# Optimization experiments

Measured on AMD Instinct MI355X. Metric: run time of the kernel, lower is better.

## Reference

```python
import jax, jax.numpy as jnp
import numpy as np
from jax.scipy.linalg import solve_triangular

CHUNK = 64

def _l2norm(x, eps=1e-6):
    return x * jax.lax.rsqrt(jnp.sum(x * x, axis=-1, keepdims=True) + eps)

def setup_inputs() -> dict:
    key = jax.random.key(0)
    ks = jax.random.split(key, 5)
    B, S, H, Dk, Dv = 2, 4096, 16, 128, 128
    query = jax.random.normal(ks[0], (B, S, H, Dk), jnp.float32)
    key_t = jax.random.normal(ks[1], (B, S, H, Dk), jnp.float32)
    value = jax.random.normal(ks[2], (B, S, H, Dv), jnp.float32)
    # g is a log-decay gate: must be <= 0 so exp(cumsum(g)) stays bounded
    g = -0.1 * jax.random.uniform(ks[3], (B, S, H), jnp.float32)
    beta = jax.random.uniform(ks[4], (B, S, H), jnp.float32)
    return {"query": query, "key": key_t, "value": value, "g": g, "beta": beta}

def reference(query, key, value, g, beta):
    """Chunked gated delta rule (faithful to torch_chunk_gated_delta_rule).
    query/key: [B,S,H,Dk], value: [B,S,H,Dv], g/beta: [B,S,H]."""
    dtype0 = query.dtype
    q = _l2norm(query).transpose(0, 2, 1, 3).astype(jnp.float32)  # [B,H,S,Dk]
    k = _l2norm(key).transpose(0, 2, 1, 3).astype(jnp.float32)
    v = value.transpose(0, 2, 1, 3).astype(jnp.float32)           # [B,H,S,Dv]
    b = beta.transpose(0, 2, 1).astype(jnp.float32)               # [B,H,S]
    gl = g.transpose(0, 2, 1).astype(jnp.float32)
    B, H, S, Dk = k.shape
    Dv = v.shape[-1]
    pad = (-S) % CHUNK
    if pad:
        q = jnp.pad(q, ((0, 0), (0, 0), (0, pad), (0, 0)))
        k = jnp.pad(k, ((0, 0), (0, 0), (0, pad), (0, 0)))
        v = jnp.pad(v, ((0, 0), (0, 0), (0, pad), (0, 0)))
        b = jnp.pad(b, ((0, 0), (0, 0), (0, pad)))
        gl = jnp.pad(gl, ((0, 0), (0, 0), (0, pad)))
    N = (S + pad) // CHUNK
    q = q * (Dk ** -0.5)
    vb = v * b[..., None]
    kb = k * b[..., None]
    qc = q.reshape(B, H, N, CHUNK, Dk)
    kc = k.reshape(B, H, N, CHUNK, Dk)
    vc = vb.reshape(B, H, N, CHUNK, Dv)
    kbc = kb.reshape(B, H, N, CHUNK, Dk)
    gc = gl.reshape(B, H, N, CHUNK)
    gcs = jnp.cumsum(gc, axis=-1)                                  # within-chunk cum log-decay
    tri = jnp.tril(jnp.ones((CHUNK, CHUNK), bool))                 # incl diag
    tri_strict = jnp.tril(jnp.ones((CHUNK, CHUNK), bool), -1)
    # decay[i,j] = exp(g_i - g_j) for i >= j else 0
    decay = jnp.where(tri, jnp.exp(jnp.where(tri, gcs[..., :, None] - gcs[..., None, :], 0.0)), 0.0)
    # Torch builds T = (I + strict_lower(k_beta k^T * decay))^{-1} via forward substitution;
    # same result from a unit-lower triangular solve.
    A = jnp.where(tri_strict, jnp.einsum('bhnck,bhndk->bhncd', kbc, kc) * decay, 0.0)
    M = A + jnp.eye(CHUNK, dtype=A.dtype)
    eye = jnp.broadcast_to(jnp.eye(CHUNK, dtype=A.dtype), M.shape)
    Tinv = solve_triangular(M, eye, lower=True, unit_diagonal=True)
    u = jnp.einsum('bhncd,bhndv->bhncv', Tinv, vc)                 # attn @ v_beta
    kcd = jnp.einsum('bhncd,bhndk->bhnck', Tinv, kbc * jnp.exp(gcs)[..., None])  # k_cumdecay

    def step(state, xs):
        q_i, k_i, u_i, kcd_i, g_i, dec_i = xs                      # [B,H,C,*]
        attn = jnp.where(tri, jnp.einsum('bhck,bhdk->bhcd', q_i, k_i) * dec_i, 0.0)
        v_new = u_i - jnp.einsum('bhck,bhkv->bhcv', kcd_i, state)
        o_i = jnp.einsum('bhck,bhkv->bhcv', q_i * jnp.exp(g_i)[..., None], state) \
            + jnp.einsum('bhcd,bhdv->bhcv', attn, v_new)
        g_last = g_i[..., -1]                                      # [B,H]
        k_dec = k_i * jnp.exp(g_last[..., None] - g_i)[..., None]
        state = state * jnp.exp(g_last)[..., None, None] \
            + jnp.einsum('bhck,bhcv->bhkv', k_dec, v_new)
        return state, o_i

    xs = tuple(jnp.moveaxis(a, 2, 0) for a in (qc, kc, u, kcd, gcs, decay))
    state0 = jnp.zeros((B, H, Dk, Dv), jnp.float32)
    _, out = jax.lax.scan(step, state0, xs)                        # out: [N,B,H,C,Dv]
    out = jnp.moveaxis(out, 0, 2).reshape(B, H, N * CHUNK, Dv)[:, :, :S]
    return out.transpose(0, 2, 1, 3).astype(dtype0)                # [B,S,H,Dv]
```

## Files before the change

### kernel.cpp

```cpp
#include <hip/hip_runtime.h>
#include <hip/hip_fp16.h>

#define B_   2
#define S_   4096
#define H_   16
#define DK_  128
#define DV_  128
#define CK_  64
#define NC_  (S_/CK_)
#define QSCALE 0.08838834764831845f

#define DOT4(a,b) ((a).x*(b).x + (a).y*(b).y + (a).z*(b).z + (a).w*(b).w)

#define SWH(c, r) (((((c) >> 3) ^ (((r) >> 2) & 7)) << 3) | ((c) & 7))
#define SWV(c, r) (((((c) >> 2) ^ (((r) >> 2) & 7)) << 2) | ((c) & 3))

static __device__ __forceinline__ unsigned short f2bf(float x) {
    unsigned u = __float_as_uint(x);
    unsigned r = u + 0x7fffu + ((u >> 16) & 1u);
    return (unsigned short)(r >> 16);
}
static __device__ __forceinline__ float bf2f(unsigned short h) {
    return __uint_as_float(((unsigned)h) << 16);
}
static __device__ __forceinline__ float4 h4tof4(const __half* p) {
    float2 f01 = __half22float2(*(const __half2*)p);
    float2 f23 = __half22float2(*(const __half2*)(p + 2));
    return make_float4(f01.x, f01.y, f23.x, f23.y);
}
static __device__ __forceinline__ void f4toh4(__half* p, float4 v) {
    *(__half2*)p       = __floats2half2_rn(v.x, v.y);
    *(__half2*)(p + 2) = __floats2half2_rn(v.z, v.w);
}

struct f8 { float4 lo, hi; };
static __device__ __forceinline__ f8 unp_bf16x8(uint4 u) {
    f8 r;
    r.lo.x = __uint_as_float(u.x << 16); r.lo.y = __uint_as_float(u.x & 0xffff0000u);
    r.lo.z = __uint_as_float(u.y << 16); r.lo.w = __uint_as_float(u.y & 0xffff0000u);
    r.hi.x = __uint_as_float(u.z << 16); r.hi.y = __uint_as_float(u.z & 0xffff0000u);
    r.hi.z = __uint_as_float(u.w << 16); r.hi.w = __uint_as_float(u.w & 0xffff0000u);
    return r;
}
static __device__ __forceinline__ f8 unp_f16x8(uint4 u) {
    f8 r;
    float2 a = __half22float2(*(__half2*)&u.x), b = __half22float2(*(__half2*)&u.y);
    float2 c = __half22float2(*(__half2*)&u.z), d = __half22float2(*(__half2*)&u.w);
    r.lo = make_float4(a.x, a.y, b.x, b.y);
    r.hi = make_float4(c.x, c.y, d.x, d.y);
    return r;
}

__global__ __launch_bounds__(256) void dr_phase1(
    const float* __restrict__ Q, const float* __restrict__ K,
    const float* __restrict__ V, const float* __restrict__ G,
    const float* __restrict__ Bt,
    unsigned short* __restrict__ Uw, unsigned short* __restrict__ KCDw,
    unsigned short* __restrict__ ATTNw,
    float* __restrict__ RQw, float* __restrict__ RKw, float* __restrict__ EGw)
{
    __shared__ float kn[64][132];
    __shared__ __align__(16) __half bufh[64][136];
    __shared__ float T[64][68];
    __shared__ float tmp[32][36];
    __shared__ float bet[64], rn[64], epos[64], eneg[64], cL[64], cR[64];

    const int tid = threadIdx.x;
    const int cid = blockIdx.x;
    const int n   = cid & (NC_ - 1);
    const int bh  = cid >> 6;
    const int h   = bh & (H_ - 1);
    const int b   = bh >> 4;
    const int rowbase = (b*S_ + n*CK_)*H_ + h;

    #pragma unroll
    for (int i = 0; i < 8; ++i) {
        int idx4 = tid + 256*i;
        int r = idx4 >> 5, c0 = (idx4 & 31) << 2;
        *(float4*)&kn[r][c0 ^ (r & 28)] =
            *(const float4*)(K + (size_t)(rowbase + r*H_)*DK_ + c0);
    }
    if (tid < 64) {
        float g = G[rowbase + tid*H_];
        #pragma unroll
        for (int off = 1; off < 64; off <<= 1) {
            float o = __shfl_up(g, off, 64);
            if (tid >= off) g += o;
        }
        float ep = expf(g);
        epos[tid] = ep;
        eneg[tid] = expf(-g);
        bet[tid]  = Bt[rowbase + tid*H_];
        if (tid == 63) EGw[cid] = ep;
    }
    __syncthreads();

    #pragma unroll
    for (int i = 0; i < 8; ++i) {
        int idx4 = tid + 256*i;
        int r = idx4 >> 5, c0 = (idx4 & 31) << 2;
        float bb = bet[r];
        float4 vv = *(const float4*)(V + (size_t)(rowbase + r*H_)*DV_ + c0);
        vv.x *= bb; vv.y *= bb; vv.z *= bb; vv.w *= bb;
        f4toh4(&bufh[r][c0], vv);
    }
    if (tid < 64) {
        const int xr = tid & 28;
        float s = 0.f;
        #pragma unroll
        for (int c = 0; c < 128; c += 4) { float4 x = *(float4*)&kn[tid][c ^ xr]; s += DOT4(x,x); }
        float r_ = rsqrtf(s + 1e-6f);
        rn[tid] = r_;
        RKw[cid*64 + tid] = r_*epos[63]*eneg[tid];
        cL[tid] = bet[tid]*epos[tid]*r_;
        cR[tid] = eneg[tid]*r_;
    }
    __syncthreads();

    {
        const int i0 = (tid >> 4) << 2, j0 = (tid & 15) << 2;
        const int xi = i0 & 28, xj = j0 & 28;
        float acc[4][4] = {};
        if (j0 <= i0) {
            for (int c = 0; c < 128; c += 4) {
                float4 a0 = *(float4*)&kn[i0  ][c ^ xi], a1 = *(float4*)&kn[i0+1][c ^ xi];
                float4 a2 = *(float4*)&kn[i0+2][c ^ xi], a3 = *(float4*)&kn[i0+3][c ^ xi];
                float4 b0 = *(float4*)&kn[j0  ][c ^ xj], b1 = *(float4*)&kn[j0+1][c ^ xj];
                float4 b2 = *(float4*)&kn[j0+2][c ^ xj], b3 = *(float4*)&kn[j0+3][c ^ xj];
                acc[0][0]+=DOT4(a0,b0); acc[0][1]+=DOT4(a0,b1); acc[0][2]+=DOT4(a0,b2); acc[0][3]+=DOT4(a0,b3);
                acc[1][0]+=DOT4(a1,b0); acc[1][1]+=DOT4(a1,b1); acc[1][2]+=DOT4(a1,b2); acc[1][3]+=DOT4(a1,b3);
                acc[2][0]+=DOT4(a2,b0); acc[2][1]+=DOT4(a2,b1); acc[2][2]+=DOT4(a2,b2); acc[2][3]+=DOT4(a2,b3);
                acc[3][0]+=DOT4(a3,b0); acc[3][1]+=DOT4(a3,b1); acc[3][2]+=DOT4(a3,b2); acc[3][3]+=DOT4(a3,b3);
            }
        }
        #pragma unroll
        for (int x = 0; x < 4; ++x) {
            float fi = cL[i0+x];
            #pragma unroll
            for (int y = 0; y < 4; ++y) {
                int i = i0+x, j = j0+y;
                T[i][j] = (i > j) ? (-fi*cR[j]*acc[x][y]) : 0.f;
            }
        }
    }
    __syncthreads();

    {
        float* tf = &tmp[0][0];
        for (int t = tid; t < 1024; t += 256) {
            int d = t >> 8, i = (t >> 4) & 15, j = t & 15;
            tf[t] = T[(d<<4) + i][(d<<4) + j];
        }
    }
    __syncthreads();
    if (tid < 64) {
        const float* Ad = &tmp[0][0] + ((tid >> 4) << 8);
        const int j = tid & 15, R = (tid >> 4) << 4;
        for (int i = j+1; i < 16; ++i) {
            float x = Ad[(i<<4) + j];
            for (int l = j+1; l < i; ++l) x += Ad[(i<<4) + l] * T[R+l][R+j];
            T[R+i][R+j] = x;
        }
    }
    __syncthreads();
    {
        const int p = tid >> 7, rem = tid & 127, i = rem >> 3, j0 = (rem & 7) << 1;
        const int bb2 = p << 5;
        float x0 = T[bb2+16+i][bb2+j0], x1 = T[bb2+16+i][bb2+j0+1];
        for (int l = j0+1; l < 16; ++l) {
            float a = T[bb2+16+i][bb2+l];
            x0 += a * T[bb2+l][bb2+j0];
            if (l > j0+1) x1 += a * T[bb2+l][bb2+j0+1];
        }
        tmp[(p<<4)+i][j0] = x0; tmp[(p<<4)+i][j0+1] = x1;
        __syncthreads();
        float y0 = tmp[(p<<4)+i][j0], y1 = tmp[(p<<4)+i][j0+1];
        for (int l = 0; l < i; ++l) {
            float a = T[bb2+16+i][bb2+16+l];
            y0 += a * tmp[(p<<4)+l][j0];
            y1 += a * tmp[(p<<4)+l][j0+1];
        }
        T[bb2+16+i][bb2+j0] = y0; T[bb2+16+i][bb2+j0+1] = y1;
    }
    __syncthreads();
    {
        const int i = tid >> 3, j0 = (tid & 7) << 2;
        float x0 = T[32+i][j0], x1 = T[32+i][j0+1], x2 = T[32+i][j0+2], x3 = T[32+i][j0+3];
        for (int l = j0+1; l < 32; ++l) {
            float a = T[32+i][l];
            x0 += a * T[l][j0];
            if (l > j0+1) x1 += a * T[l][j0+1];
            if (l > j0+2) x2 += a * T[l][j0+2];
            if (l > j0+3) x3 += a * T[l][j0+3];
        }
        tmp[i][j0] = x0; tmp[i][j0+1] = x1; tmp[i][j0+2] = x2; tmp[i][j0+3] = x3;
        __syncthreads();
        float y0 = tmp[i][j0], y1 = tmp[i][j0+1], y2 = tmp[i][j0+2], y3 = tmp[i][j0+3];
        for (int l = 0; l < i; ++l) {
            float a = T[32+i][32+l];
            y0 += a * tmp[l][j0];   y1 += a * tmp[l][j0+1];
            y2 += a * tmp[l][j0+2]; y3 += a * tmp[l][j0+3];
        }
        T[32+i][j0] = y0; T[32+i][j0+1] = y1; T[32+i][j0+2] = y2; T[32+i][j0+3] = y3;
    }
    __syncthreads();

    {
        unsigned short* Up = Uw + (size_t)cid*(CK_*DV_);
        for (int tt = tid; tt < 512; tt += 256) {
            const int i0 = (tt >> 5) << 2, c0 = (tt & 31) << 2;
            float4 acc[4];
            #pragma unroll
            for (int x = 0; x < 4; ++x) acc[x] = h4tof4(&bufh[i0+x][c0]);
            for (int j0 = 0; j0 <= i0; j0 += 4) {
                float4 t0 = *(float4*)&T[i0][j0],   t1 = *(float4*)&T[i0+1][j0];
                float4 t2 = *(float4*)&T[i0+2][j0], t3 = *(float4*)&T[i0+3][j0];
                float4 b0 = h4tof4(&bufh[j0][c0]),   b1 = h4tof4(&bufh[j0+1][c0]);
                float4 b2 = h4tof4(&bufh[j0+2][c0]), b3 = h4tof4(&bufh[j0+3][c0]);
                acc[0].x += t0.x*b0.x + t0.y*b1.x + t0.z*b2.x + t0.w*b3.x;
                acc[0].y += t0.x*b0.y + t0.y*b1.y + t0.z*b2.y + t0.w*b3.y;
                acc[0].z += t0.x*b0.z + t0.y*b1.z + t0.z*b2.z + t0.w*b3.z;
                acc[0].w += t0.x*b0.w + t0.y*b1.w + t0.z*b2.w + t0.w*b3.w;
                acc[1].x += t1.x*b0.x + t1.y*b1.x + t1.z*b2.x + t1.w*b3.x;
                acc[1].y += t1.x*b0.y + t1.y*b1.y + t1.z*b2.y + t1.w*b3.y;
                acc[1].z += t1.x*b0.z + t1.y*b1.z + t1.z*b2.z + t1.w*b3.z;
                acc[1].w += t1.x*b0.w + t1.y*b1.w + t1.z*b2.w + t1.w*b3.w;
                acc[2].x += t2.x*b0.x + t2.y*b1.x + t2.z*b2.x + t2.w*b3.x;
                acc[2].y += t2.x*b0.y + t2.y*b1.y + t2.z*b2.y + t2.w*b3.y;
                acc[2].z += t2.x*b0.z + t2.y*b1.z + t2.z*b2.z + t2.w*b3.z;
                acc[2].w += t2.x*b0.w + t2.y*b1.w + t2.z*b2.w + t2.w*b3.w;
                acc[3].x += t3.x*b0.x + t3.y*b1.x + t3.z*b2.x + t3.w*b3.x;
                acc[3].y += t3.x*b0.y + t3.y*b1.y + t3.z*b2.y + t3.w*b3.y;
                acc[3].z += t3.x*b0.z + t3.y*b1.z + t3.z*b2.z + t3.w*b3.z;
                acc[3].w += t3.x*b0.w + t3.y*b1.w + t3.z*b2.w + t3.w*b3.w;
            }
            #pragma unroll
            for (int x = 0; x < 4; ++x) {
                ushort4 o; o.x = f2bf(acc[x].x); o.y = f2bf(acc[x].y);
                o.z = f2bf(acc[x].z); o.w = f2bf(acc[x].w);
                *(ushort4*)(Up + (i0+x)*DV_ + c0) = o;
            }
        }
        unsigned short* Kp = KCDw + (size_t)cid*(CK_*DK_);
        for (int tt = tid; tt < 512; tt += 256) {
            const int i0 = (tt >> 5) << 2, c0 = (tt & 31) << 2;
            const int xi = i0 & 28;
            float4 acc[4];
            #pragma unroll
            for (int x = 0; x < 4; ++x) {
                float wi = cL[i0+x];
                float4 kv = *(float4*)&kn[i0+x][c0 ^ xi];
                acc[x].x = kv.x*wi; acc[x].y = kv.y*wi; acc[x].z = kv.z*wi; acc[x].w = kv.w*wi;
            }
            for (int j0 = 0; j0 <= i0; j0 += 4) {
                const int xj = j0 & 28;
                float w0 = cL[j0], w1 = cL[j0+1], w2 = cL[j0+2], w3 = cL[j0+3];
                float4 t0 = *(float4*)&T[i0][j0],   t1 = *(float4*)&T[i0+1][j0];
                float4 t2 = *(float4*)&T[i0+2][j0], t3 = *(float4*)&T[i0+3][j0];
                float4 b0 = *(float4*)&kn[j0  ][c0 ^ xj], b1 = *(float4*)&kn[j0+1][c0 ^ xj];
                float4 b2 = *(float4*)&kn[j0+2][c0 ^ xj], b3 = *(float4*)&kn[j0+3][c0 ^ xj];
                b0.x*=w0; b0.y*=w0; b0.z*=w0; b0.w*=w0;
                b1.x*=w1; b1.y*=w1; b1.z*=w1; b1.w*=w1;
                b2.x*=w2; b2.y*=w2; b2.z*=w2; b2.w*=w2;
                b3.x*=w3; b3.y*=w3; b3.z*=w3; b3.w*=w3;
                acc[0].x += t0.x*b0.x + t0.y*b1.x + t0.z*b2.x + t0.w*b3.x;
                acc[0].y += t0.x*b0.y + t0.y*b1.y + t0.z*b2.y + t0.w*b3.y;
                acc[0].z += t0.x*b0.z + t0.y*b1.z + t0.z*b2.z + t0.w*b3.z;
                acc[0].w += t0.x*b0.w + t0.y*b1.w + t0.z*b2.w + t0.w*b3.w;
                acc[1].x += t1.x*b0.x + t1.y*b1.x + t1.z*b2.x + t1.w*b3.x;
                acc[1].y += t1.x*b0.y + t1.y*b1.y + t1.z*b2.y + t1.w*b3.y;
                acc[1].z += t1.x*b0.z + t1.y*b1.z + t1.z*b2.z + t1.w*b3.z;
                acc[1].w += t1.x*b0.w + t1.y*b1.w + t1.z*b2.w + t1.w*b3.w;
                acc[2].x += t2.x*b0.x + t2.y*b1.x + t2.z*b2.x + t2.w*b3.x;
                acc[2].y += t2.x*b0.y + t2.y*b1.y + t2.z*b2.y + t2.w*b3.y;
                acc[2].z += t2.x*b0.z + t2.y*b1.z + t2.z*b2.z + t2.w*b3.z;
                acc[2].w += t2.x*b0.w + t2.y*b1.w + t2.z*b2.w + t2.w*b3.w;
                acc[3].x += t3.x*b0.x + t3.y*b1.x + t3.z*b2.x + t3.w*b3.x;
                acc[3].y += t3.x*b0.y + t3.y*b1.y + t3.z*b2.y + t3.w*b3.y;
                acc[3].z += t3.x*b0.z + t3.y*b1.z + t3.z*b2.z + t3.w*b3.z;
                acc[3].w += t3.x*b0.w + t3.y*b1.w + t3.z*b2.w + t3.w*b3.w;
            }
            #pragma unroll
            for (int x = 0; x < 4; ++x) {
                ushort4 o; o.x = f2bf(acc[x].x); o.y = f2bf(acc[x].y);
                o.z = f2bf(acc[x].z); o.w = f2bf(acc[x].w);
                *(ushort4*)(Kp + (i0+x)*DK_ + c0) = o;
            }
        }
    }
    __syncthreads();

    #pragma unroll
    for (int i = 0; i < 8; ++i) {
        int idx4 = tid + 256*i;
        int r = idx4 >> 5, c0 = (idx4 & 31) << 2;
        f4toh4(&bufh[r][c0], *(const float4*)(Q + (size_t)(rowbase + r*H_)*DK_ + c0));
    }
    __syncthreads();
    if (tid < 64) {
        float s = 0.f;
        #pragma unroll
        for (int c = 0; c < 128; c += 4) { float4 x = h4tof4(&bufh[tid][c]); s += DOT4(x,x); }
        float r_ = rsqrtf(s + 1e-6f)*QSCALE;
        rn[tid] = r_;
        RQw[cid*64 + tid] = r_*epos[tid];
    }
    __syncthreads();

    {
        unsigned short* Ap = ATTNw + (size_t)cid*(CK_*CK_);
        const int i0 = (tid >> 4) << 2, j0 = (tid & 15) << 2;
        const int xj = j0 & 28;
        float acc[4][4] = {};
        if (j0 <= i0) {
            for (int c = 0; c < 128; c += 4) {
                float4 a0 = h4tof4(&bufh[i0  ][c]), a1 = h4tof4(&bufh[i0+1][c]);
                float4 a2 = h4tof4(&bufh[i0+2][c]), a3 = h4tof4(&bufh[i0+3][c]);
                float4 b0 = *(float4*)&kn[j0  ][c ^ xj], b1 = *(float4*)&kn[j0+1][c ^ xj];
                float4 b2 = *(float4*)&kn[j0+2][c ^ xj], b3 = *(float4*)&kn[j0+3][c ^ xj];
                acc[0][0]+=DOT4(a0,b0); acc[0][1]+=DOT4(a0,b1); acc[0][2]+=DOT4(a0,b2); acc[0][3]+=DOT4(a0,b3);
                acc[1][0]+=DOT4(a1,b0); acc[1][1]+=DOT4(a1,b1); acc[1][2]+=DOT4(a1,b2); acc[1][3]+=DOT4(a1,b3);
                acc[2][0]+=DOT4(a2,b0); acc[2][1]+=DOT4(a2,b1); acc[2][2]+=DOT4(a2,b2); acc[2][3]+=DOT4(a2,b3);
                acc[3][0]+=DOT4(a3,b0); acc[3][1]+=DOT4(a3,b1); acc[3][2]+=DOT4(a3,b2); acc[3][3]+=DOT4(a3,b3);
            }
        }
        #pragma unroll
        for (int x = 0; x < 4; ++x) {
            ushort4 o;
            int i = i0+x;
            float fi = rn[i]*epos[i];
            float v0 = (j0   <= i) ? acc[x][0]*fi*cR[j0]   : 0.f;
            float v1 = (j0+1 <= i) ? acc[x][1]*fi*cR[j0+1] : 0.f;
            float v2 = (j0+2 <= i) ? acc[x][2]*fi*cR[j0+2] : 0.f;
            float v3 = (j0+3 <= i) ? acc[x][3]*fi*cR[j0+3] : 0.f;
            o.x = f2bf(v0); o.y = f2bf(v1); o.z = f2bf(v2); o.w = f2bf(v3);
            *(ushort4*)(Ap + i*CK_ + j0) = o;
        }
    }
}

#define P2_LOAD(nn) do { \
    const int cid_ = bh*NC_ + (nn); \
    const int rb_ = (b*S_ + (nn)*CK_)*H_ + h; \
    _Pragma("unroll") \
    for (int i = 0; i < 4; ++i) { \
        int idx4 = tid + 512*i; \
        int r = idx4 >> 5; \
        pk[i]  = *(const float4*)(K + (size_t)(rb_ + r*H_)*DK_ + ((idx4 & 31)*4)); \
        pc[i]  = ((const uint2*)(KCDw + (size_t)cid_*8192))[idx4]; \
        prk[i] = RKw[cid_*64 + r]; \
    } \
    pu = *(const unsigned*)(Uw + (size_t)cid_*8192 + lane*128 + v0 + 2*w); \
} while(0)

__global__ __launch_bounds__(512) void dr_phase2(
    const float* __restrict__ K,
    const unsigned short* __restrict__ Uw, const unsigned short* __restrict__ KCDw,
    const float* __restrict__ RKw, const float* __restrict__ EGw,
    unsigned short* __restrict__ STw)
{
    __shared__ __align__(16) unsigned short kch[2][64][136];
    __shared__ float kd[2][64][132];
    __shared__ float stT[16][132];
    __shared__ float vnw[8][64][2];

    const int tid = threadIdx.x;
    const int bidx = blockIdx.x;
    const int xcd  = bidx & 7;
    const int slot = bidx >> 3;
    const int vs   = slot >> 2;
    const int bh   = ((slot & 3) << 3) | xcd;
    const int h = bh & (H_-1), b = bh >> 4;
    const int v0 = vs*16;
    const int w = tid >> 6, lane = tid & 63;
    const int lva = 2*w, lvb = 2*w + 1;
    const int c2 = 2*lane;

    float2 sA = {0.f, 0.f}, sB = {0.f, 0.f};
    *(float2*)&stT[lva][c2] = sA;
    *(float2*)&stT[lvb][c2] = sB;

    float4 pk[4]; uint2 pc[4]; float prk[4]; unsigned pu;
    P2_LOAD(0);

    int cur = 0;
    for (int n = 0; n < NC_; ++n) {
        const int cid = bh*NC_ + n;
        const float u0 = bf2f((unsigned short)(pu & 0xffff));
        const float u1 = bf2f((unsigned short)(pu >> 16));

        #pragma unroll
        for (int i = 0; i < 4; ++i) {
            int idx4 = tid + 512*i;
            int r = idx4 >> 5, c0 = (idx4 & 31)*4;
            *(uint2*)&kch[cur][r][SWH(c0, r)] = pc[i];
            float4 kv = pk[i];
            kv.x *= prk[i]; kv.y *= prk[i]; kv.z *= prk[i]; kv.w *= prk[i];
            *(float4*)&kd[cur][r][c0] = kv;
        }
        if (n+1 < NC_) P2_LOAD(n+1);
        __syncthreads();

        {
            unsigned pA = (unsigned)f2bf(sA.x) | ((unsigned)f2bf(sA.y) << 16);
            unsigned pB = (unsigned)f2bf(sB.x) | ((unsigned)f2bf(sB.y) << 16);
            size_t base = ((size_t)cid*128 + v0)*128;
            *(unsigned*)(STw + base + (size_t)lva*128 + c2) = pA;
            *(unsigned*)(STw + base + (size_t)lvb*128 + c2) = pB;
        }

        float vA = u0, vB = u1;
        for (int k0 = 0; k0 < 128; k0 += 8) {
            f8 a = unp_bf16x8(*(const uint4*)&kch[cur][lane][SWH(k0, lane)]);
            float4 pa0 = *(const float4*)&stT[lva][k0], pa1 = *(const float4*)&stT[lva][k0+4];
            float4 pb0 = *(const float4*)&stT[lvb][k0], pb1 = *(const float4*)&stT[lvb][k0+4];
            vA -= DOT4(a.lo, pa0) + DOT4(a.hi, pa1);
            vB -= DOT4(a.lo, pb0) + DOT4(a.hi, pb1);
        }
        vnw[w][lane][0] = vA;
        vnw[w][lane][1] = vB;

        const float a_dec = EGw[cid];
        sA.x *= a_dec; sA.y *= a_dec; sB.x *= a_dec; sB.y *= a_dec;
        for (int r = 0; r < 64; ++r) {
            float2 vv = *(const float2*)&vnw[w][r];
            float2 kv = *(const float2*)&kd[cur][r][c2];
            sA.x += vv.x*kv.x; sA.y += vv.x*kv.y;
            sB.x += vv.y*kv.x; sB.y += vv.y*kv.y;
        }
        *(float2*)&stT[lva][c2] = sA;
        *(float2*)&stT[lvb][c2] = sB;

        cur ^= 1;
    }
}

__global__ __launch_bounds__(256) void dr_phase3(
    const float* __restrict__ Q,
    const unsigned short* __restrict__ Uw, const unsigned short* __restrict__ KCDw,
    const unsigned short* __restrict__ ATTNw, const unsigned short* __restrict__ STw,
    const float* __restrict__ RQw, float* __restrict__ Out)
{
    __shared__ __align__(16) __half         qh[64][136];
    __shared__ __align__(16) unsigned short kch[64][136];
    __shared__ __align__(16) unsigned short sth[64][136];
    __shared__ __align__(16) unsigned short ath[64][72];
    __shared__ float vnT[64][68];

    const int tid = threadIdx.x;
    const int bidx = blockIdx.x;
    const int xcd  = bidx & 7;
    const int half = (bidx >> 3) & 1;
    const int cid  = ((bidx >> 4) << 3) | xcd;
    const int n = cid & (NC_-1), bh = cid >> 6;
    const int h = bh & (H_-1), b = bh >> 4;
    const int rowbase = (b*S_ + n*CK_)*H_ + h;
    const int vbase = half*64;

    #pragma unroll
    for (int i = 0; i < 8; ++i) {
        int idx4 = tid + 256*i;
        int r = idx4 >> 5, c0 = (idx4 & 31)*4;
        float rq = RQw[cid*64 + r];
        float4 qv = *(const float4*)(Q + (size_t)(rowbase + r*H_)*DK_ + c0);
        qv.x *= rq; qv.y *= rq; qv.z *= rq; qv.w *= rq;
        f4toh4(&qh[r][SWH(c0, r)], qv);
        uint2 kcv = ((const uint2*)(KCDw + (size_t)cid*8192))[idx4];
        *(uint2*)&kch[r][SWH(c0, r)] = kcv;
        uint2 stv = ((const uint2*)(STw + ((size_t)cid*128 + vbase)*128))[idx4];
        *(uint2*)&sth[r][SWH(c0, r)] = stv;
    }
    #pragma unroll
    for (int i = 0; i < 4; ++i) {
        int idx4 = tid + 256*i;
        int r = idx4 >> 4, j0 = (idx4 & 15)*4;
        uint2 av = ((const uint2*)(ATTNw + (size_t)cid*4096))[idx4];
        *(uint2*)&ath[r][SWH(j0, r)] = av;
    }
    __syncthreads();

    const int r0 = (tid >> 4)*4, v4 = (tid & 15)*4;

    {
        float4 acc[4];
        #pragma unroll
        for (int x = 0; x < 4; ++x) {
            ushort4 uv = *(const ushort4*)(Uw + (size_t)cid*8192 + (r0+x)*128 + vbase + v4);
            acc[x].x = bf2f(uv.x); acc[x].y = bf2f(uv.y); acc[x].z = bf2f(uv.z); acc[x].w = bf2f(uv.w);
        }
        for (int k0 = 0; k0 < 128; k0 += 8) {
            f8 A[4], Bv[4];
            #pragma unroll
            for (int x = 0; x < 4; ++x) A[x]  = unp_bf16x8(*(const uint4*)&kch[r0+x][SWH(k0, r0+x)]);
            #pragma unroll
            for (int y = 0; y < 4; ++y) Bv[y] = unp_bf16x8(*(const uint4*)&sth[v4+y][SWH(k0, v4+y)]);
            #pragma unroll
            for (int x = 0; x < 4; ++x) {
                acc[x].x -= DOT4(A[x].lo, Bv[0].lo) + DOT4(A[x].hi, Bv[0].hi);
                acc[x].y -= DOT4(A[x].lo, Bv[1].lo) + DOT4(A[x].hi, Bv[1].hi);
                acc[x].z -= DOT4(A[x].lo, Bv[2].lo) + DOT4(A[x].hi, Bv[2].hi);
                acc[x].w -= DOT4(A[x].lo, Bv[3].lo) + DOT4(A[x].hi, Bv[3].hi);
            }
        }
        #pragma unroll
        for (int x = 0; x < 4; ++x) {
            vnT[v4+0][SWV(r0+x, v4+0)] = acc[x].x;
            vnT[v4+1][SWV(r0+x, v4+1)] = acc[x].y;
            vnT[v4+2][SWV(r0+x, v4+2)] = acc[x].z;
            vnT[v4+3][SWV(r0+x, v4+3)] = acc[x].w;
        }
    }
    __syncthreads();

    {
        float4 acc[4] = {};
        for (int k0 = 0; k0 < 128; k0 += 8) {
            f8 A[4], Bv[4];
            #pragma unroll
            for (int x = 0; x < 4; ++x) A[x]  = unp_f16x8(*(const uint4*)&qh[r0+x][SWH(k0, r0+x)]);
            #pragma unroll
            for (int y = 0; y < 4; ++y) Bv[y] = unp_bf16x8(*(const uint4*)&sth[v4+y][SWH(k0, v4+y)]);
            #pragma unroll
            for (int x = 0; x < 4; ++x) {
                acc[x].x += DOT4(A[x].lo, Bv[0].lo) + DOT4(A[x].hi, Bv[0].hi);
                acc[x].y += DOT4(A[x].lo, Bv[1].lo) + DOT4(A[x].hi, Bv[1].hi);
                acc[x].z += DOT4(A[x].lo, Bv[2].lo) + DOT4(A[x].hi, Bv[2].hi);
                acc[x].w += DOT4(A[x].lo, Bv[3].lo) + DOT4(A[x].hi, Bv[3].hi);
            }
        }
        for (int j0 = 0; j0 <= r0+3; j0 += 8) {
            f8 A[4];
            #pragma unroll
            for (int x = 0; x < 4; ++x) A[x] = unp_bf16x8(*(const uint4*)&ath[r0+x][SWH(j0, r0+x)]);
            float4 bLo[4], bHi[4];
            #pragma unroll
            for (int y = 0; y < 4; ++y) {
                bLo[y] = *(const float4*)&vnT[v4+y][SWV(j0,   v4+y)];
                bHi[y] = *(const float4*)&vnT[v4+y][SWV(j0+4, v4+y)];
            }
            #pragma unroll
            for (int x = 0; x < 4; ++x) {
                acc[x].x += DOT4(A[x].lo, bLo[0]) + DOT4(A[x].hi, bHi[0]);
                acc[x].y += DOT4(A[x].lo, bLo[1]) + DOT4(A[x].hi, bHi[1]);
                acc[x].z += DOT4(A[x].lo, bLo[2]) + DOT4(A[x].hi, bHi[2]);
                acc[x].w += DOT4(A[x].lo, bLo[3]) + DOT4(A[x].hi, bHi[3]);
            }
        }
        #pragma unroll
        for (int x = 0; x < 4; ++x)
            *(float4*)(Out + (size_t)(rowbase + (r0+x)*H_)*DV_ + vbase + v4) = acc[x];
    }
}

extern "C" void kernel_launch(void* const* d_in, const int* in_sizes, int n_in,
                              void* d_out, int out_size, void* d_ws, size_t ws_size,
                              hipStream_t stream) {
    (void)in_sizes; (void)n_in; (void)out_size; (void)ws_size;
    const float* Q  = (const float*)d_in[0];
    const float* K  = (const float*)d_in[1];
    const float* V  = (const float*)d_in[2];
    const float* G  = (const float*)d_in[3];
    const float* Bt = (const float*)d_in[4];
    float* Out = (float*)d_out;

    unsigned short* Uw    = (unsigned short*)d_ws;
    unsigned short* KCDw  = Uw    + (size_t)2048*64*128;
    unsigned short* ATTNw = KCDw  + (size_t)2048*64*128;
    unsigned short* STw   = ATTNw + (size_t)2048*64*64;
    float* RQw = (float*)(STw + (size_t)2048*128*128);
    float* RKw = RQw + 2048*64;
    float* EGw = RKw + 2048*64;

    dr_phase1<<<2048, 256, 0, stream>>>(Q, K, V, G, Bt, Uw, KCDw, ATTNw, RQw, RKw, EGw);
    dr_phase2<<<256, 512, 0, stream>>>(K, Uw, KCDw, RKw, EGw, STw);
    dr_phase3<<<4096, 256, 0, stream>>>(Q, Uw, KCDw, ATTNw, STw, RQw, Out);
}
```

Baseline: 806.2 us.

## Use bf16 MFMA for phase-3 chunk matmuls instead of scalar FMA

Replaces the scalar fp32 dot-product loops in the output phase with 16x16x32 bf16 MFMA instructions. The query is staged in bf16 rather than fp16, the intermediate v_new is stored as bf16 in shared memory, and the KCD sign is flipped on load so the subtraction becomes an accumulate. Each wave now owns 16 rows and the causal attention product skips k-slices above the diagonal. This removes most of the ALU cost of phase 3, at the price of lower precision for q and v_new and scattered scalar output stores.

```diff
diff --git a/kernel.cpp b/kernel.cpp
--- a/kernel.cpp
+++ b/kernel.cpp
@@ -15,6 +15,9 @@
 #define SWH(c, r) (((((c) >> 3) ^ (((r) >> 2) & 7)) << 3) | ((c) & 7))
 #define SWV(c, r) (((((c) >> 2) ^ (((r) >> 2) & 7)) << 2) | ((c) & 3))
 
+typedef __attribute__((ext_vector_type(8))) short bf16x8;
+typedef __attribute__((ext_vector_type(4))) float f32x4;
+
 static __device__ __forceinline__ unsigned short f2bf(float x) {
     unsigned u = __float_as_uint(x);
     unsigned r = u + 0x7fffu + ((u >> 16) & 1u);
@@ -40,14 +43,6 @@
     r.lo.z = __uint_as_float(u.y << 16); r.lo.w = __uint_as_float(u.y & 0xffff0000u);
     r.hi.x = __uint_as_float(u.z << 16); r.hi.y = __uint_as_float(u.z & 0xffff0000u);
     r.hi.z = __uint_as_float(u.w << 16); r.hi.w = __uint_as_float(u.w & 0xffff0000u);
-    return r;
-}
-static __device__ __forceinline__ f8 unp_f16x8(uint4 u) {
-    f8 r;
-    float2 a = __half22float2(*(__half2*)&u.x), b = __half22float2(*(__half2*)&u.y);
-    float2 c = __half22float2(*(__half2*)&u.z), d = __half22float2(*(__half2*)&u.w);
-    r.lo = make_float4(a.x, a.y, b.x, b.y);
-    r.hi = make_float4(c.x, c.y, d.x, d.y);
     return r;
 }
 
@@ -441,11 +436,11 @@
     const unsigned short* __restrict__ ATTNw, const unsigned short* __restrict__ STw,
     const float* __restrict__ RQw, float* __restrict__ Out)
 {
-    __shared__ __align__(16) __half         qh[64][136];
+    __shared__ __align__(16) unsigned short qbh[64][136];
     __shared__ __align__(16) unsigned short kch[64][136];
     __shared__ __align__(16) unsigned short sth[64][136];
     __shared__ __align__(16) unsigned short ath[64][72];
-    __shared__ float vnT[64][68];
+    __shared__ __align__(16) unsigned short vnbh[64][72];
 
     const int tid = threadIdx.x;
     const int bidx = blockIdx.x;
@@ -457,15 +452,34 @@
     const int rowbase = (b*S_ + n*CK_)*H_ + h;
     const int vbase = half*64;
 
+    const int w = tid >> 6, l = tid & 63;
+    const int R = w*16;
+    const int lrow = l & 15;
+    const int lk = (l >> 4) * 8;
+    const int lreg4 = (l >> 4) * 4;
+
+    float uval[4][4];
+    {
+        const unsigned short* up = Uw + (size_t)cid*8192 + (R + lreg4)*128 + vbase + lrow;
+        #pragma unroll
+        for (int vt = 0; vt < 4; ++vt)
+            #pragma unroll
+            for (int rg = 0; rg < 4; ++rg)
+                uval[vt][rg] = bf2f(up[rg*128 + vt*16]);
+    }
+
     #pragma unroll
     for (int i = 0; i < 8; ++i) {
         int idx4 = tid + 256*i;
         int r = idx4 >> 5, c0 = (idx4 & 31)*4;
         float rq = RQw[cid*64 + r];
         float4 qv = *(const float4*)(Q + (size_t)(rowbase + r*H_)*DK_ + c0);
-        qv.x *= rq; qv.y *= rq; qv.z *= rq; qv.w *= rq;
-        f4toh4(&qh[r][SWH(c0, r)], qv);
+        ushort4 qo;
+        qo.x = f2bf(qv.x*rq); qo.y = f2bf(qv.y*rq);
+        qo.z = f2bf(qv.z*rq); qo.w = f2bf(qv.w*rq);
+        *(ushort4*)&qbh[r][SWH(c0, r)] = qo;
         uint2 kcv = ((const uint2*)(KCDw + (size_t)cid*8192))[idx4];
+        kcv.x ^= 0x80008000u; kcv.y ^= 0x80008000u;
         *(uint2*)&kch[r][SWH(c0, r)] = kcv;
         uint2 stv = ((const uint2*)(STw + ((size_t)cid*128 + vbase)*128))[idx4];
         *(uint2*)&sth[r][SWH(c0, r)] = stv;
@@ -479,77 +493,60 @@
     }
     __syncthreads();
 
-    const int r0 = (tid >> 4)*4, v4 = (tid & 15)*4;
-
-    {
-        float4 acc[4];
-        #pragma unroll
-        for (int x = 0; x < 4; ++x) {
-            ushort4 uv = *(const ushort4*)(Uw + (size_t)cid*8192 + (r0+x)*128 + vbase + v4);
-            acc[x].x = bf2f(uv.x); acc[x].y = bf2f(uv.y); acc[x].z = bf2f(uv.z); acc[x].w = bf2f(uv.w);
-        }
-        for (int k0 = 0; k0 < 128; k0 += 8) {
-            f8 A[4], Bv[4];
-            #pragma unroll
-            for (int x = 0; x < 4; ++x) A[x]  = unp_bf16x8(*(const uint4*)&kch[r0+x][SWH(k0, r0+x)]);
-            #pragma unroll
-            for (int y = 0; y < 4; ++y) Bv[y] = unp_bf16x8(*(const uint4*)&sth[v4+y][SWH(k0, v4+y)]);
-            #pragma unroll
-            for (int x = 0; x < 4; ++x) {
-                acc[x].x -= DOT4(A[x].lo, Bv[0].lo) + DOT4(A[x].hi, Bv[0].hi);
-                acc[x].y -= DOT4(A[x].lo, Bv[1].lo) + DOT4(A[x].hi, Bv[1].hi);
-                acc[x].z -= DOT4(A[x].lo, Bv[2].lo) + DOT4(A[x].hi, Bv[2].hi);
-                acc[x].w -= DOT4(A[x].lo, Bv[3].lo) + DOT4(A[x].hi, Bv[3].hi);
-            }
-        }
-        #pragma unroll
-        for (int x = 0; x < 4; ++x) {
-            vnT[v4+0][SWV(r0+x, v4+0)] = acc[x].x;
-            vnT[v4+1][SWV(r0+x, v4+1)] = acc[x].y;
-            vnT[v4+2][SWV(r0+x, v4+2)] = acc[x].z;
-            vnT[v4+3][SWV(r0+x, v4+3)] = acc[x].w;
-        }
-    }
-    __syncthreads();
-
-    {
-        float4 acc[4] = {};
-        for (int k0 = 0; k0 < 128; k0 += 8) {
-            f8 A[4], Bv[4];
-            #pragma unroll
-            for (int x = 0; x < 4; ++x) A[x]  = unp_f16x8(*(const uint4*)&qh[r0+x][SWH(k0, r0+x)]);
-            #pragma unroll
-            for (int y = 0; y < 4; ++y) Bv[y] = unp_bf16x8(*(const uint4*)&sth[v4+y][SWH(k0, v4+y)]);
-            #pragma unroll
-            for (int x = 0; x < 4; ++x) {
-                acc[x].x += DOT4(A[x].lo, Bv[0].lo) + DOT4(A[x].hi, Bv[0].hi);
-                acc[x].y += DOT4(A[x].lo, Bv[1].lo) + DOT4(A[x].hi, Bv[1].hi);
-                acc[x].z += DOT4(A[x].lo, Bv[2].lo) + DOT4(A[x].hi, Bv[2].hi);
-                acc[x].w += DOT4(A[x].lo, Bv[3].lo) + DOT4(A[x].hi, Bv[3].hi);
-            }
-        }
-        for (int j0 = 0; j0 <= r0+3; j0 += 8) {
-            f8 A[4];
-            #pragma unroll
-            for (int x = 0; x < 4; ++x) A[x] = unp_bf16x8(*(const uint4*)&ath[r0+x][SWH(j0, r0+x)]);
-            float4 bLo[4], bHi[4];
-            #pragma unroll
-            for (int y = 0; y < 4; ++y) {
-                bLo[y] = *(const float4*)&vnT[v4+y][SWV(j0,   v4+y)];
-                bHi[y] = *(const float4*)&vnT[v4+y][SWV(j0+4, v4+y)];
-            }
-            #pragma unroll
-            for (int x = 0; x < 4; ++x) {
-                acc[x].x += DOT4(A[x].lo, bLo[0]) + DOT4(A[x].hi, bHi[0]);
-                acc[x].y += DOT4(A[x].lo, bLo[1]) + DOT4(A[x].hi, bHi[1]);
-                acc[x].z += DOT4(A[x].lo, bLo[2]) + DOT4(A[x].hi, bHi[2]);
-                acc[x].w += DOT4(A[x].lo, bLo[3]) + DOT4(A[x].hi, bHi[3]);
-            }
-        }
-        #pragma unroll
-        for (int x = 0; x < 4; ++x)
-            *(float4*)(Out + (size_t)(rowbase + (r0+x)*H_)*DV_ + vbase + v4) = acc[x];
-    }
+    f32x4 vac[4];
+    #pragma unroll
+    for (int vt = 0; vt < 4; ++vt) {
+        vac[vt][0] = uval[vt][0]; vac[vt][1] = uval[vt][1];
+        vac[vt][2] = uval[vt][2]; vac[vt][3] = uval[vt][3];
+    }
+    #pragma unroll
+    for (int ks = 0; ks < 4; ++ks) {
+        bf16x8 a = *(const bf16x8*)&kch[R + lrow][SWH(ks*32 + lk, R + lrow)];
+        #pragma unroll
+        for (int vt = 0; vt < 4; ++vt) {
+            bf16x8 bb = *(const bf16x8*)&sth[vt*16 + lrow][SWH(ks*32 + lk, vt*16 + lrow)];
+            vac[vt] = __builtin_amdgcn_mfma_f32_16x16x32_bf16(a, bb, vac[vt], 0, 0, 0);
+        }
+    }
+    #pragma unroll
+    for (int vt = 0; vt < 4; ++vt) {
+        ushort4 o;
+        o.x = f2bf(vac[vt][0]); o.y = f2bf(vac[vt][1]);
+        o.z = f2bf(vac[vt][2]); o.w = f2bf(vac[vt][3]);
+        *(ushort4*)&vnbh[vt*16 + lrow][SWH(R + lreg4, vt*16 + lrow)] = o;
+    }
+    __syncthreads();
+
+    f32x4 oac[4];
+    const f32x4 zero4 = {0.f, 0.f, 0.f, 0.f};
+    #pragma unroll
+    for (int vt = 0; vt < 4; ++vt) oac[vt] = zero4;
+    #pragma unroll
+    for (int ks = 0; ks < 4; ++ks) {
+        bf16x8 a = *(const bf16x8*)&qbh[R + lrow][SWH(ks*32 + lk, R + lrow)];
+        #pragma unroll
+        for (int vt = 0; vt < 4; ++vt) {
+            bf16x8 bb = *(const bf16x8*)&sth[vt*16 + lrow][SWH(ks*32 + lk, vt*16 + lrow)];
+            oac[vt] = __builtin_amdgcn_mfma_f32_16x16x32_bf16(a, bb, oac[vt], 0, 0, 0);
+        }
+    }
+    const int nka = (w < 2) ? 1 : 2;
+    for (int ks = 0; ks < nka; ++ks) {
+        bf16x8 a = *(const bf16x8*)&ath[R + lrow][SWH(ks*32 + lk, R + lrow)];
+        #pragma unroll
+        for (int vt = 0; vt < 4; ++vt) {
+            bf16x8 bb = *(const bf16x8*)&vnbh[vt*16 + lrow][SWH(ks*32 + lk, vt*16 + lrow)];
+            oac[vt] = __builtin_amdgcn_mfma_f32_16x16x32_bf16(a, bb, oac[vt], 0, 0, 0);
+        }
+    }
+
+    #pragma unroll
+    for (int vt = 0; vt < 4; ++vt)
+        #pragma unroll
+        for (int rg = 0; rg < 4; ++rg) {
+            int row = R + lreg4 + rg;
+            Out[(size_t)(rowbase + row*H_)*DV_ + vbase + vt*16 + lrow] = oac[vt][rg];
+        }
 }
 
 extern "C" void kernel_launch(void* const* d_in, const int* in_sizes, int n_in,
```

Measured after the change: 668.9 us. -17.0%, faster.
